# Kernel tuning notes

Hardware: AMD Instinct MI355X
Metric: run time of the kernel (lower is better)

The kernel has to match this reference:

```python
import jax, jax.numpy as jnp
import numpy as np

HEAD_SIZE = 64
EMBED = 1024


def setup_inputs() -> dict:
    key = jax.random.key(0)
    k1, k2, k3, k4 = jax.random.split(key, 4)
    B, T, D = 4, 4096, EMBED
    x = jax.random.normal(k1, (B, T, D), dtype=jnp.float32)
    # nn.Linear weights: [out_features, in_features]
    Wk = jax.random.normal(k2, (HEAD_SIZE, D), dtype=jnp.float32) * (D ** -0.5)
    Wq = jax.random.normal(k3, (HEAD_SIZE, D), dtype=jnp.float32) * (D ** -0.5)
    Wv = jax.random.normal(k4, (D, D), dtype=jnp.float32) * (D ** -0.5)
    return {"x": x, "Wk": Wk, "Wq": Wq, "Wv": Wv}


def reference(x, Wk, Wq, Wv):
    # x: [B, T, D]
    B, T, D = x.shape
    K = jnp.einsum('btd,hd->bth', x, Wk)      # [B, T, H]
    Q = jnp.einsum('btd,hd->bth', x, Wq)      # [B, T, H]
    V = jnp.einsum('btd,ed->bte', x, Wv)      # [B, T, D]
    scale = 1.0 / jnp.sqrt(jnp.float32(HEAD_SIZE))
    scores = jnp.einsum('bth,bsh->bts', Q, K) * scale  # [B, T, T]
    causal = jnp.tril(jnp.ones((T, T), dtype=bool))
    scores = jnp.where(causal, scores, jnp.float32(-jnp.inf))
    attn = jax.nn.softmax(scores, axis=-1)
    out = jnp.einsum('bts,bse->bte', attn, V)  # [B, T, D]
    return out
```

## Files before the change

kernel.cpp:

```cpp
#include <hip/hip_runtime.h>
#include <hip/hip_bf16.h>


typedef __attribute__((ext_vector_type(8))) short bf16x8;
typedef __attribute__((ext_vector_type(4))) float f32x4;

typedef unsigned short u16;
typedef unsigned int u32;

__device__ inline u16 f2bf(float f) {
    u32 u = __builtin_bit_cast(u32, f);
    u = (u + 0x7fff + ((u >> 16) & 1)) >> 16;
    return (u16)u;
}

__device__ inline u32 pkbf(float a, float b) {
    return (u32)f2bf(a) | ((u32)f2bf(b) << 16);
}

__device__ inline void g2lds16(const void* g, void* l) {
    __builtin_amdgcn_global_load_lds(
        (const __attribute__((address_space(1))) unsigned int*)g,
        (__attribute__((address_space(3))) unsigned int*)l, 16, 0, 0);
}


__global__ void cvt_x(const float* __restrict__ src, u16* __restrict__ dst,
                      int n) {
    const int i = (blockIdx.x * blockDim.x + threadIdx.x) * 8;
    if (i + 7 < n) {
        const float4 a = *(const float4*)(src + i);
        const float4 b = *(const float4*)(src + i + 4);
        u32 r[4];
        r[0] = pkbf(a.x, a.y);
        r[1] = pkbf(a.z, a.w);
        r[2] = pkbf(b.x, b.y);
        r[3] = pkbf(b.z, b.w);
        *(uint4*)(dst + i) = *(const uint4*)r;
    }
}

__global__ void cvt_w(const float* __restrict__ Wk, const float* __restrict__ Wq,
                      const float* __restrict__ Wv,
                      u16* __restrict__ Wkb, u16* __restrict__ Wqb,
                      u16* __restrict__ Wvb, float qscale) {
    const int i = (blockIdx.x * blockDim.x + threadIdx.x) * 8;
    const float* src; u16* dst; int j; float s = 1.0f;
    if (i < 65536)        { src = Wk; dst = Wkb; j = i; }
    else if (i < 131072)  { src = Wq; dst = Wqb; j = i - 65536; s = qscale; }
    else                  { src = Wv; dst = Wvb; j = i - 131072; }
    const float4 a = *(const float4*)(src + j);
    const float4 b = *(const float4*)(src + j + 4);
    u32 r[4];
    r[0] = pkbf(a.x * s, a.y * s);
    r[1] = pkbf(a.z * s, a.w * s);
    r[2] = pkbf(b.x * s, b.y * s);
    r[3] = pkbf(b.z * s, b.w * s);
    *(uint4*)(dst + j) = *(const uint4*)r;
}

template <int MODE>
__device__ __forceinline__ void gemm_body(
    int m0, int n0,
    const u16* __restrict__ A,
    const u16* __restrict__ B0, const u16* __restrict__ B1, int nsplit,
    u16* __restrict__ D0, u16* __restrict__ D1,
    u16* Alds, u16* Blds)
{
    const int tid  = threadIdx.x;
    const int lane = tid & 63, w = tid >> 6;
    const int quad = lane >> 4, l15 = lane & 15;
    const int wr = w >> 1, wc = w & 1;
    const int mrow0 = wr * 64, ncol0 = wc * 64;

    f32x4 acc[4][4] = {};

    const int srow = (lane >> 3);
    const int scol = (lane & 7) * 8;

    for (int k0 = 0; k0 < 1024; k0 += 64) {
        __syncthreads();
#pragma unroll
        for (int c = 0; c < 4; ++c) {
            const int chunk = c * 4 + w;
            const int row = chunk * 8 + srow;
            const u16* ga = A + (size_t)(m0 + row) * 1024 + k0 + scol;
            g2lds16(ga, &Alds[chunk * 512]);
            const int brow = n0 + row;
            const u16* gb = (brow < nsplit ? B0 + (size_t)brow * 1024
                                           : B1 + (size_t)(brow - nsplit) * 1024)
                            + k0 + scol;
            g2lds16(gb, &Blds[chunk * 512]);
        }
        __syncthreads();

#pragma unroll
        for (int kk = 0; kk < 64; kk += 32) {
            bf16x8 af[4], bfr[4];
#pragma unroll
            for (int mb = 0; mb < 4; ++mb)
                af[mb] = *(const bf16x8*)&Alds[(mrow0 + mb * 16 + l15) * 64 + kk + quad * 8];
#pragma unroll
            for (int nb = 0; nb < 4; ++nb)
                bfr[nb] = *(const bf16x8*)&Blds[(ncol0 + nb * 16 + l15) * 64 + kk + quad * 8];
#pragma unroll
            for (int mb = 0; mb < 4; ++mb)
#pragma unroll
                for (int nb = 0; nb < 4; ++nb)
                    acc[mb][nb] = __builtin_amdgcn_mfma_f32_16x16x32_bf16(
                        af[mb], bfr[nb], acc[mb][nb], 0, 0, 0);
        }
    }

#pragma unroll
    for (int mb = 0; mb < 4; ++mb)
#pragma unroll
        for (int nb = 0; nb < 4; ++nb)
#pragma unroll
            for (int r = 0; r < 4; ++r) {
                const int row = m0 + mrow0 + mb * 16 + quad * 4 + r;
                const int col = n0 + ncol0 + nb * 16 + l15;
                const u16 v = f2bf(acc[mb][nb][r]);
                if (MODE == 1) {
                    const int h = col & 63;
                    u16* dst = (col < 64) ? D0 : D1;
                    const size_t idx = (size_t)((row >> 4) * 2 + (h >> 5)) * 512
                                     + ((row & 15) + ((h >> 3) & 3) * 16) * 8
                                     + (h & 7);
                    dst[idx] = v;
                } else {
                    const size_t idx = (size_t)((row >> 4) * 512 + (col >> 5)) * 512
                                     + ((row & 15) + ((col >> 3) & 3) * 16) * 8
                                     + (col & 7);
                    D0[idx] = v;
                }
            }
}

__global__ __launch_bounds__(256, 2) void gemm_all(
    const u16* __restrict__ xb,
    const u16* __restrict__ Wqb, const u16* __restrict__ Wkb,
    const u16* __restrict__ Wvb,
    u16* __restrict__ Qf, u16* __restrict__ Kf, u16* __restrict__ Vf)
{
    __shared__ u16 Alds[128 * 64];
    __shared__ u16 Blds[128 * 64];
    const int d = blockIdx.x;
    if (d < 128) {
        gemm_body<1>(d * 128, 0, xb, Wqb, Wkb, 64, Qf, Kf, Alds, Blds);
    } else {
        const int dd = d - 128;
        gemm_body<2>((dd >> 7) * 128, (dd & 127) * 128, Wvb, xb, xb, 1 << 30,
                     Vf, nullptr, Alds, Blds);
    }
}

__global__ __launch_bounds__(512, 4) void attn_fa(
    const u16* __restrict__ Qf,
    const u16* __restrict__ Kf,
    const u16* __restrict__ Vf,
    float* __restrict__ Out)
{
    __shared__ u16 Vlds[2][16 * 512];
    __shared__ u16 Plds[2][128 * 40];

    const int tid  = threadIdx.x;
    const int lane = tid & 63, w = tid >> 6;
    const int quad = lane >> 4, l15 = lane & 15;

    const int d  = blockIdx.y * 128 + blockIdx.x;
    const int g  = d >> 4;
    const int qt = (g < 16) ? (31 - g) : (g - 16);
    const int e0 = ((d >> 2) & 3) * 256;
    const int b  = d & 3;
    const int bt0 = b * 4096;

    const int qs = w >> 1, es = w & 1;
    const int qrow0 = qt * 128 + qs * 32;

    bf16x8 qf[2][2];
#pragma unroll
    for (int mb = 0; mb < 2; ++mb)
#pragma unroll
        for (int kk = 0; kk < 2; ++kk) {
            const int btile = (bt0 + qrow0 + mb * 16) >> 4;
            qf[mb][kk] = *(const bf16x8*)&Qf[(size_t)(btile * 2 + kk) * 512 + lane * 8];
        }

    const short o = (short)0x3F80;
    const bf16x8 ones = {o, o, o, o, o, o, o, o};

    f32x4 acc[2][8] = {};
    f32x4 accl[2]  = {};

    const int ntiles = 4 * qt + 4;
    const int qlim = qrow0 + 31;

    auto stageV = [&](int buf, int it) {
        const int stile = (bt0 + it * 32) >> 5;
#pragma unroll
        for (int t2 = 0; t2 < 2; ++t2) {
            const int t = w * 2 + t2;
            g2lds16(&Vf[(size_t)(((e0 >> 4) + t) * 512 + stile) * 512 + lane * 8],
                    &Vlds[buf][t * 512]);
        }
    };

    auto loadK = [&](int jt, bf16x8* kf) {
#pragma unroll
        for (int kk = 0; kk < 2; ++kk) {
            const int kt = ((bt0 + jt * 32 + es * 16) >> 4) * 2 + kk;
            kf[kk] = *(const bf16x8*)&Kf[(size_t)kt * 512 + lane * 8];
        }
    };

    auto computeP = [&](int jt, const bf16x8* kf) {
        const int s0 = jt * 32;
        f32x4 sf[2] = {};
#pragma unroll
        for (int mb = 0; mb < 2; ++mb)
#pragma unroll
            for (int kk = 0; kk < 2; ++kk)
                sf[mb] = __builtin_amdgcn_mfma_f32_16x16x32_bf16(
                    qf[mb][kk], kf[kk], sf[mb], 0, 0, 0);
        if (s0 + 31 > qrow0) {
            const int colabs = s0 + es * 16 + l15;
#pragma unroll
            for (int mb = 0; mb < 2; ++mb)
#pragma unroll
                for (int r = 0; r < 4; ++r) {
                    const int rowabs = qrow0 + mb * 16 + quad * 4 + r;
                    sf[mb][r] = (colabs <= rowabs) ? sf[mb][r] : -__builtin_inff();
                }
        }
        u16* Pl = &Plds[jt & 1][(qs * 32 + quad * 4) * 40 + es * 16 + l15];
#pragma unroll
        for (int mb = 0; mb < 2; ++mb) {
            const u32 p01 = pkbf(exp2f(sf[mb][0]), exp2f(sf[mb][1]));
            const u32 p23 = pkbf(exp2f(sf[mb][2]), exp2f(sf[mb][3]));
            u16* base = Pl + mb * 16 * 40;
            base[0]      = (u16)p01;
            base[40]     = (u16)(p01 >> 16);
            base[80]     = (u16)p23;
            base[120]    = (u16)(p23 >> 16);
        }
    };

    stageV(0, 0);
    {
        bf16x8 kf0[2];
        loadK(0, kf0);
        computeP(0, kf0);
    }

    for (int it = 0; it < ntiles; ++it) {
        __syncthreads();
        const int buf = it & 1;
        const bool haveNext = (it + 1 < ntiles);
        const bool nextActive = haveNext && ((it + 1) * 32 <= qlim);
        const bool curActive = (it * 32 <= qlim);

        if (haveNext) stageV(buf ^ 1, it + 1);
        bf16x8 kf[2];
        if (nextActive) loadK(it + 1, kf);

        if (curActive) {
            bf16x8 pf[2];
#pragma unroll
            for (int mb = 0; mb < 2; ++mb)
                pf[mb] = *(const bf16x8*)&Plds[buf][(qs * 32 + mb * 16 + l15) * 40 + quad * 8];
#pragma unroll
            for (int mb = 0; mb < 2; ++mb)
                accl[mb] = __builtin_amdgcn_mfma_f32_16x16x32_bf16(
                    pf[mb], ones, accl[mb], 0, 0, 0);
#pragma unroll
            for (int nb = 0; nb < 8; ++nb) {
                bf16x8 vf = *(const bf16x8*)&Vlds[buf][(es * 8 + nb) * 512 + lane * 8];
#pragma unroll
                for (int mb = 0; mb < 2; ++mb)
                    acc[mb][nb] = __builtin_amdgcn_mfma_f32_16x16x32_bf16(
                        pf[mb], vf, acc[mb][nb], 0, 0, 0);
            }
        }

        if (nextActive) computeP(it + 1, kf);
    }

    float rl[2][4];
#pragma unroll
    for (int mb = 0; mb < 2; ++mb)
#pragma unroll
        for (int r = 0; r < 4; ++r) rl[mb][r] = 1.0f / accl[mb][r];
#pragma unroll
    for (int mb = 0; mb < 2; ++mb)
#pragma unroll
        for (int nb = 0; nb < 8; ++nb)
#pragma unroll
            for (int r = 0; r < 4; ++r) {
                const int row = qrow0 + mb * 16 + quad * 4 + r;
                const int col = e0 + es * 128 + nb * 16 + l15;
                Out[(size_t)(bt0 + row) * 1024 + col] = acc[mb][nb][r] * rl[mb][r];
            }
}

extern "C" void kernel_launch(void* const* d_in, const int* in_sizes, int n_in,
                              void* d_out, int out_size, void* d_ws, size_t ws_size,
                              hipStream_t stream) {
    const float* x  = (const float*)d_in[0];
    const float* Wk = (const float*)d_in[1];
    const float* Wq = (const float*)d_in[2];
    const float* Wv = (const float*)d_in[3];

    const int nx  = in_sizes[0];
    const int nwk = in_sizes[1];
    const int nwq = in_sizes[2];
    const int nwv = in_sizes[3];

    u16* xb  = (u16*)d_ws;
    u16* Wkb = xb  + (size_t)nx;
    u16* Wqb = Wkb + (size_t)nwk;
    u16* Wvb = Wqb + (size_t)nwq;
    u16* Qf  = Wvb + (size_t)nwv;
    u16* Kf  = Qf  + (size_t)1024 * 2 * 512;
    u16* Vf  = Kf  + (size_t)1024 * 2 * 512;
    float* out = (float*)d_out;

    const float qscale = 0.125f * 1.44269504088896f;

    cvt_x<<<nx / 2048, 256, 0, stream>>>(x, xb, nx);
    cvt_w<<<(nwk + nwq + nwv) / 2048, 256, 0, stream>>>(Wk, Wq, Wv,
                                                        Wkb, Wqb, Wvb, qscale);

    gemm_all<<<1152, 256, 0, stream>>>(xb, Wqb, Wkb, Wvb, Qf, Kf, Vf);

    attn_fa<<<dim3(128, 4), 512, 0, stream>>>(Qf, Kf, Vf, out);
}
```

Baseline: 347.4 us.

## Split attention block across 16 waves with 16 query rows each

Doubles the attention block from 512 to 1024 threads so each wave owns 16 query rows instead of 32, halving the per-wave accumulators and MFMA work per K/V tile. V staging now uses one load per wave instead of two. The goal is more waves in flight and lower register pressure to hide latency. In exchange, each loaded V fragment from LDS is reused by only one MFMA instead of two, and barrier cost rises with more waves per block.

```diff
diff --git a/kernel.cpp b/kernel.cpp
--- a/kernel.cpp
+++ b/kernel.cpp
@@ -155,7 +155,7 @@
     }
 }
 
-__global__ __launch_bounds__(512, 4) void attn_fa(
+__global__ __launch_bounds__(1024, 4) void attn_fa(
     const u16* __restrict__ Qf,
     const u16* __restrict__ Kf,
     const u16* __restrict__ Vf,
@@ -176,34 +176,29 @@
     const int bt0 = b * 4096;
 
     const int qs = w >> 1, es = w & 1;
-    const int qrow0 = qt * 128 + qs * 32;
-
-    bf16x8 qf[2][2];
-#pragma unroll
-    for (int mb = 0; mb < 2; ++mb)
-#pragma unroll
-        for (int kk = 0; kk < 2; ++kk) {
-            const int btile = (bt0 + qrow0 + mb * 16) >> 4;
-            qf[mb][kk] = *(const bf16x8*)&Qf[(size_t)(btile * 2 + kk) * 512 + lane * 8];
-        }
+    const int qrow0 = qt * 128 + qs * 16;
+
+    bf16x8 qf[2];
+    {
+        const int btile = (bt0 + qrow0) >> 4;
+#pragma unroll
+        for (int kk = 0; kk < 2; ++kk)
+            qf[kk] = *(const bf16x8*)&Qf[(size_t)(btile * 2 + kk) * 512 + lane * 8];
+    }
 
     const short o = (short)0x3F80;
     const bf16x8 ones = {o, o, o, o, o, o, o, o};
 
-    f32x4 acc[2][8] = {};
-    f32x4 accl[2]  = {};
+    f32x4 acc[8] = {};
+    f32x4 accl = {};
 
     const int ntiles = 4 * qt + 4;
-    const int qlim = qrow0 + 31;
+    const int qlim = qrow0 + 15;
 
     auto stageV = [&](int buf, int it) {
         const int stile = (bt0 + it * 32) >> 5;
-#pragma unroll
-        for (int t2 = 0; t2 < 2; ++t2) {
-            const int t = w * 2 + t2;
-            g2lds16(&Vf[(size_t)(((e0 >> 4) + t) * 512 + stile) * 512 + lane * 8],
-                    &Vlds[buf][t * 512]);
-        }
+        g2lds16(&Vf[(size_t)(((e0 >> 4) + w) * 512 + stile) * 512 + lane * 8],
+                &Vlds[buf][w * 512]);
     };
 
     auto loadK = [&](int jt, bf16x8* kf) {
@@ -216,34 +211,25 @@
 
     auto computeP = [&](int jt, const bf16x8* kf) {
         const int s0 = jt * 32;
-        f32x4 sf[2] = {};
-#pragma unroll
-        for (int mb = 0; mb < 2; ++mb)
-#pragma unroll
-            for (int kk = 0; kk < 2; ++kk)
-                sf[mb] = __builtin_amdgcn_mfma_f32_16x16x32_bf16(
-                    qf[mb][kk], kf[kk], sf[mb], 0, 0, 0);
+        f32x4 sf = {};
+#pragma unroll
+        for (int kk = 0; kk < 2; ++kk)
+            sf = __builtin_amdgcn_mfma_f32_16x16x32_bf16(qf[kk], kf[kk], sf, 0, 0, 0);
         if (s0 + 31 > qrow0) {
             const int colabs = s0 + es * 16 + l15;
 #pragma unroll
-            for (int mb = 0; mb < 2; ++mb)
-#pragma unroll
-                for (int r = 0; r < 4; ++r) {
-                    const int rowabs = qrow0 + mb * 16 + quad * 4 + r;
-                    sf[mb][r] = (colabs <= rowabs) ? sf[mb][r] : -__builtin_inff();
-                }
-        }
-        u16* Pl = &Plds[jt & 1][(qs * 32 + quad * 4) * 40 + es * 16 + l15];
-#pragma unroll
-        for (int mb = 0; mb < 2; ++mb) {
-            const u32 p01 = pkbf(exp2f(sf[mb][0]), exp2f(sf[mb][1]));
-            const u32 p23 = pkbf(exp2f(sf[mb][2]), exp2f(sf[mb][3]));
-            u16* base = Pl + mb * 16 * 40;
-            base[0]      = (u16)p01;
-            base[40]     = (u16)(p01 >> 16);
-            base[80]     = (u16)p23;
-            base[120]    = (u16)(p23 >> 16);
-        }
+            for (int r = 0; r < 4; ++r) {
+                const int rowabs = qrow0 + quad * 4 + r;
+                sf[r] = (colabs <= rowabs) ? sf[r] : -__builtin_inff();
+            }
+        }
+        u16* Pl = &Plds[jt & 1][(qs * 16 + quad * 4) * 40 + es * 16 + l15];
+        const u32 p01 = pkbf(exp2f(sf[0]), exp2f(sf[1]));
+        const u32 p23 = pkbf(exp2f(sf[2]), exp2f(sf[3]));
+        Pl[0]   = (u16)p01;
+        Pl[40]  = (u16)(p01 >> 16);
+        Pl[80]  = (u16)p23;
+        Pl[120] = (u16)(p23 >> 16);
     };
 
     stageV(0, 0);
@@ -265,42 +251,30 @@
         if (nextActive) loadK(it + 1, kf);
 
         if (curActive) {
-            bf16x8 pf[2];
-#pragma unroll
-            for (int mb = 0; mb < 2; ++mb)
-                pf[mb] = *(const bf16x8*)&Plds[buf][(qs * 32 + mb * 16 + l15) * 40 + quad * 8];
-#pragma unroll
-            for (int mb = 0; mb < 2; ++mb)
-                accl[mb] = __builtin_amdgcn_mfma_f32_16x16x32_bf16(
-                    pf[mb], ones, accl[mb], 0, 0, 0);
+            const bf16x8 pf = *(const bf16x8*)&Plds[buf][(qs * 16 + l15) * 40 + quad * 8];
+            accl = __builtin_amdgcn_mfma_f32_16x16x32_bf16(pf, ones, accl, 0, 0, 0);
 #pragma unroll
             for (int nb = 0; nb < 8; ++nb) {
                 bf16x8 vf = *(const bf16x8*)&Vlds[buf][(es * 8 + nb) * 512 + lane * 8];
-#pragma unroll
-                for (int mb = 0; mb < 2; ++mb)
-                    acc[mb][nb] = __builtin_amdgcn_mfma_f32_16x16x32_bf16(
-                        pf[mb], vf, acc[mb][nb], 0, 0, 0);
+                acc[nb] = __builtin_amdgcn_mfma_f32_16x16x32_bf16(
+                    pf, vf, acc[nb], 0, 0, 0);
             }
         }
 
         if (nextActive) computeP(it + 1, kf);
     }
 
-    float rl[2][4];
-#pragma unroll
-    for (int mb = 0; mb < 2; ++mb)
-#pragma unroll
-        for (int r = 0; r < 4; ++r) rl[mb][r] = 1.0f / accl[mb][r];
-#pragma unroll
-    for (int mb = 0; mb < 2; ++mb)
-#pragma unroll
-        for (int nb = 0; nb < 8; ++nb)
-#pragma unroll
-            for (int r = 0; r < 4; ++r) {
-                const int row = qrow0 + mb * 16 + quad * 4 + r;
-                const int col = e0 + es * 128 + nb * 16 + l15;
-                Out[(size_t)(bt0 + row) * 1024 + col] = acc[mb][nb][r] * rl[mb][r];
-            }
+    float rl[4];
+#pragma unroll
+    for (int r = 0; r < 4; ++r) rl[r] = 1.0f / accl[r];
+#pragma unroll
+    for (int nb = 0; nb < 8; ++nb)
+#pragma unroll
+        for (int r = 0; r < 4; ++r) {
+            const int row = qrow0 + quad * 4 + r;
+            const int col = e0 + es * 128 + nb * 16 + l15;
+            Out[(size_t)(bt0 + row) * 1024 + col] = acc[nb][r] * rl[r];
+        }
 }
 
 extern "C" void kernel_launch(void* const* d_in, const int* in_sizes, int n_in,
@@ -333,5 +307,5 @@
 
     gemm_all<<<1152, 256, 0, stream>>>(xb, Wqb, Wkb, Wvb, Qf, Kf, Vf);
 
-    attn_fa<<<dim3(128, 4), 512, 0, stream>>>(Qf, Kf, Vf, out);
-}
+    attn_fa<<<dim3(128, 4), 1024, 0, stream>>>(Qf, Kf, Vf, out);
+}
```

New measurement: 355.5 us. 2.3% more time.
